# Kernel tuning notes

Measured on AMD Instinct MI355X. Metric: run time of the kernel, lower is better.

The kernel has to match this reference:

```python
import jax, jax.numpy as jnp
import numpy as np

N_NODES = 50000
N_EDGES = 1_600_000
DIMS = [512, 2048, 1024, 512]  # input, hiddens..., output
NEG_SLOPE = 0.2
EPS = 1e-12


def setup_inputs() -> dict:
    key = jax.random.key(0)
    ks = jax.random.split(key, 12)
    inp = {
        "x": jax.random.normal(ks[0], (N_NODES, DIMS[0]), dtype=jnp.float32),
        "edge_row": jax.random.randint(ks[1], (N_EDGES,), 0, N_NODES, dtype=jnp.int32),
        "edge_col": jax.random.randint(ks[2], (N_EDGES,), 0, N_NODES, dtype=jnp.int32),
        "edge_val": jax.random.uniform(ks[3], (N_EDGES,), dtype=jnp.float32),
    }
    # GraphConvolution params per layer: W [d_in, d_out], b [d_out]
    for i in range(len(DIMS) - 1):
        d_in, d_out = DIMS[i], DIMS[i + 1]
        scale = 1.0 / np.sqrt(d_in)
        inp[f"W{i}"] = jax.random.uniform(ks[4 + 2 * i], (d_in, d_out), minval=-scale, maxval=scale, dtype=jnp.float32)
        inp[f"b{i}"] = jnp.zeros((d_out,), dtype=jnp.float32)
    return inp


def _spmm(edge_row, edge_col, edge_val, h):
    # out[i] = sum_{e: row[e]==i} val[e] * h[col[e]]   (sparse adj @ h)
    msgs = edge_val[:, None] * h[edge_col]  # [E, d]
    return jax.ops.segment_sum(msgs, edge_row, num_segments=N_NODES)


def reference(x, edge_row, edge_col, edge_val, W0, b0, W1, b1, W2, b2):
    Ws = [W0, W1, W2]
    bs = [b0, b1, b2]
    # F.normalize: L2-normalize each row
    norm = jnp.sqrt(jnp.sum(x * x, axis=1, keepdims=True))
    h = x / jnp.maximum(norm, EPS)
    n_layers = len(Ws)
    for i in range(n_layers):
        support = h @ Ws[i]                                  # [N, d_out]
        h = _spmm(edge_row, edge_col, edge_val, support) + bs[i]
        if i != n_layers - 1:
            # dropout is identity at inference; leaky_relu(0.2)
            h = jnp.where(h >= 0, h, NEG_SLOPE * h)
    return h
```

## Files before the change

### kernel.cpp

```cpp
#include <hip/hip_runtime.h>
#include <stdint.h>

#define N_NODES 50000
#define N_EDGES 1600000
#define NCB 13

typedef __attribute__((ext_vector_type(8))) short bf16x8;
typedef __attribute__((ext_vector_type(4))) float f32x4;
typedef __attribute__((ext_vector_type(8))) unsigned short u16x8;

__device__ __forceinline__ float b2f(unsigned short u) {
  union { unsigned int i; float f; } v; v.i = ((unsigned int)u) << 16; return v.f;
}
__device__ __forceinline__ unsigned short f2b(float f) {
  union { float f; unsigned int i; } v; v.f = f;
  unsigned int u = v.i;
  u += 0x7fffu + ((u >> 16) & 1u);
  return (unsigned short)(u >> 16);
}

__device__ __forceinline__ void load_lds16(const void* g, void* l) {
  __builtin_amdgcn_global_load_lds(
      (const __attribute__((address_space(1))) unsigned int*)g,
      (__attribute__((address_space(3))) unsigned int*)l, 16, 0, 0);
}

__global__ __launch_bounds__(256) void normalize_k(const float* __restrict__ x,
                                                   unsigned short* __restrict__ out) {
  int lane = threadIdx.x & 63;
  int row = blockIdx.x * 4 + (threadIdx.x >> 6);
  const float* p = x + (size_t)row * 512 + lane * 8;
  float4 a = ((const float4*)p)[0];
  float4 b = ((const float4*)p)[1];
  float ss = a.x*a.x + a.y*a.y + a.z*a.z + a.w*a.w
           + b.x*b.x + b.y*b.y + b.z*b.z + b.w*b.w;
#pragma unroll
  for (int off = 1; off < 64; off <<= 1) ss += __shfl_xor(ss, off, 64);
  float s = 1.0f / fmaxf(sqrtf(ss), 1e-12f);
  u16x8 o;
  o[0]=f2b(a.x*s); o[1]=f2b(a.y*s); o[2]=f2b(a.z*s); o[3]=f2b(a.w*s);
  o[4]=f2b(b.x*s); o[5]=f2b(b.y*s); o[6]=f2b(b.z*s); o[7]=f2b(b.w*s);
  *(u16x8*)(out + (size_t)row * 512 + lane * 8) = o;
}

__global__ __launch_bounds__(256) void hist2_k(const int* __restrict__ er, const int* __restrict__ ec,
                                               int* __restrict__ h2) {
  int i = blockIdx.x * 256 + threadIdx.x;
  if (i < N_EDGES) atomicAdd(&h2[er[i] * NCB + (ec[i] >> 12)], 1);
}

__global__ __launch_bounds__(256) void scan1_k(const int* __restrict__ deg, int* __restrict__ out,
                                               int* __restrict__ csum, int n) {
  __shared__ int sd[256];
  int t = threadIdx.x;
  int base = blockIdx.x * 1024;
  int v[4], s = 0;
#pragma unroll
  for (int j = 0; j < 4; ++j) {
    int idx = base + t * 4 + j;
    v[j] = (idx < n) ? deg[idx] : 0;
    s += v[j];
  }
  sd[t] = s;
  __syncthreads();
  for (int off = 1; off < 256; off <<= 1) {
    int xx = (t >= off) ? sd[t - off] : 0;
    __syncthreads();
    sd[t] += xx;
    __syncthreads();
  }
  if (t == 255) csum[blockIdx.x] = sd[255];
  int run = sd[t] - s;
#pragma unroll
  for (int j = 0; j < 4; ++j) {
    int idx = base + t * 4 + j;
    if (idx < n) out[idx] = run;
    run += v[j];
  }
}

__global__ __launch_bounds__(256) void scan2p_k(int* __restrict__ csum, int n) {
  __shared__ int sd[256];
  int t = threadIdx.x;
  int v[3], s = 0;
#pragma unroll
  for (int j = 0; j < 3; ++j) {
    int idx = t * 3 + j;
    v[j] = (idx < n) ? csum[idx] : 0;
    s += v[j];
  }
  sd[t] = s;
  __syncthreads();
  for (int off = 1; off < 256; off <<= 1) {
    int xx = (t >= off) ? sd[t - off] : 0;
    __syncthreads();
    sd[t] += xx;
    __syncthreads();
  }
  int run = sd[t] - s;
#pragma unroll
  for (int j = 0; j < 3; ++j) {
    int idx = t * 3 + j;
    if (idx < n) csum[idx] = run;
    run += v[j];
  }
}

__global__ __launch_bounds__(256) void scan3_k(int* __restrict__ out, const int* __restrict__ csum, int n) {
  int i = blockIdx.x * 256 + threadIdx.x;
  if (i < n) out[i] += csum[i >> 10];
}

__global__ __launch_bounds__(256) void extract_k(const int* __restrict__ rs2, int* __restrict__ rs_s) {
  int i = blockIdx.x * 256 + threadIdx.x;
  if (i < N_NODES) rs_s[i] = rs2[i * NCB];
  if (i == N_NODES) rs_s[i] = N_EDGES;
}

__global__ __launch_bounds__(256) void scatter2_k(const int* __restrict__ er, const int* __restrict__ ec,
    const float* __restrict__ ev, int* __restrict__ head2, int2* __restrict__ ep) {
  int i = blockIdx.x * 256 + threadIdx.x;
  if (i < N_EDGES) {
    int r = er[i], c = ec[i];
    int p = atomicAdd(&head2[r * NCB + (c >> 12)], 1);
    ep[p] = make_int2(c, __float_as_int(ev[i]));
  }
}

__global__ __launch_bounds__(256) void wconv_k(const float* __restrict__ W,
                                               unsigned short* __restrict__ WT, int K, int N) {
  int i = blockIdx.x * 256 + threadIdx.x;
  if (i < N * K) {
    int n = i / K, k = i - n * K;
    WT[i] = f2b(W[(size_t)k * N + n]);
  }
}

template <int D, int MODE>
__global__ __launch_bounds__(256) void spmm_k(const unsigned short* __restrict__ in,
    const int* __restrict__ rs, const int2* __restrict__ ep,
    const float* __restrict__ bias, void* __restrict__ outv) {
  constexpr int NS = D / 512;
  int lane = threadIdx.x & 63;
  int blk = blockIdx.x;
  int slice = (NS == 1) ? 0 : (blk / 12500);
  int rowg = (NS == 1) ? blk : (blk - slice * 12500);
  int row = rowg * 4 + (threadIdx.x >> 6);
  int e0 = rs[row];
  int e1 = rs[row + 1];
  float acc[8] = {0.f, 0.f, 0.f, 0.f, 0.f, 0.f, 0.f, 0.f};
  const unsigned short* base = in + (size_t)slice * 512 + (size_t)lane * 8;
  int e = e0;
  for (; e + 4 <= e1; e += 4) {
    int2 p0 = ep[e];
    int2 p1 = ep[e + 1];
    int2 p2 = ep[e + 2];
    int2 p3 = ep[e + 3];
    unsigned c0 = (unsigned)p0.x < N_NODES ? (unsigned)p0.x : 0u;
    unsigned c1 = (unsigned)p1.x < N_NODES ? (unsigned)p1.x : 0u;
    unsigned c2 = (unsigned)p2.x < N_NODES ? (unsigned)p2.x : 0u;
    unsigned c3 = (unsigned)p3.x < N_NODES ? (unsigned)p3.x : 0u;
    u16x8 u0 = *(const u16x8*)(base + (size_t)c0 * D);
    u16x8 u1 = *(const u16x8*)(base + (size_t)c1 * D);
    u16x8 u2 = *(const u16x8*)(base + (size_t)c2 * D);
    u16x8 u3 = *(const u16x8*)(base + (size_t)c3 * D);
    float v0 = __int_as_float(p0.y), v1 = __int_as_float(p1.y);
    float v2 = __int_as_float(p2.y), v3 = __int_as_float(p3.y);
#pragma unroll
    for (int h = 0; h < 8; ++h) acc[h] = fmaf(v0, b2f(u0[h]), acc[h]);
#pragma unroll
    for (int h = 0; h < 8; ++h) acc[h] = fmaf(v1, b2f(u1[h]), acc[h]);
#pragma unroll
    for (int h = 0; h < 8; ++h) acc[h] = fmaf(v2, b2f(u2[h]), acc[h]);
#pragma unroll
    for (int h = 0; h < 8; ++h) acc[h] = fmaf(v3, b2f(u3[h]), acc[h]);
  }
  for (; e < e1; ++e) {
    int2 p = ep[e];
    unsigned c = (unsigned)p.x < N_NODES ? (unsigned)p.x : 0u;
    u16x8 u = *(const u16x8*)(base + (size_t)c * D);
    float v = __int_as_float(p.y);
#pragma unroll
    for (int h = 0; h < 8; ++h) acc[h] = fmaf(v, b2f(u[h]), acc[h]);
  }
  size_t obase = (size_t)row * D + (size_t)slice * 512 + lane * 8;
  int bbase = slice * 512 + lane * 8;
  if (MODE == 2) {
    float* out = (float*)outv;
#pragma unroll
    for (int j = 0; j < 8; ++j) out[obase + j] = acc[j] + bias[bbase + j];
  } else {
    unsigned short* out = (unsigned short*)outv;
    u16x8 o;
#pragma unroll
    for (int h = 0; h < 8; ++h) {
      float xo = acc[h];
      if (MODE == 1) {
        xo += bias[bbase + h];
        xo = xo >= 0.f ? xo : 0.2f * xo;
      }
      o[h] = f2b(xo);
    }
    *(u16x8*)(out + obase) = o;
  }
}

template <bool BIAS_RELU>
__global__ __launch_bounds__(256) void gemm_bt_k(
    const unsigned short* __restrict__ A, const unsigned short* __restrict__ BT,
    const float* __restrict__ bias, unsigned short* __restrict__ C,
    int M, int N, int K) {
  __shared__ __align__(16) unsigned short sA[128 * 32];
  __shared__ __align__(16) unsigned short sB[128 * 32];
  int tid = threadIdx.x;
  int lane = tid & 63;
  int wid = tid >> 6;
  int wm = (wid & 1) * 64;
  int wn = (wid >> 1) * 64;
  int mblk = blockIdx.y * 128;
  int nblk = blockIdx.x * 128;
  const unsigned short* Bb = BT + (size_t)nblk * K;
  int c0 = tid, c1 = tid + 256;
  int ar0 = c0 >> 2, ac0 = (c0 & 3) * 8;
  int ar1 = c1 >> 2, ac1 = (c1 & 3) * 8;
  int ra0 = mblk + ar0; if (ra0 > M - 1) ra0 = M - 1;
  int ra1 = mblk + ar1; if (ra1 > M - 1) ra1 = M - 1;
  f32x4 acc[4][4] = {};
  for (int k0 = 0; k0 < K; k0 += 32) {
    load_lds16(A + (size_t)ra0 * K + k0 + ac0, &sA[c0 * 8]);
    load_lds16(A + (size_t)ra1 * K + k0 + ac1, &sA[c1 * 8]);
    load_lds16(Bb + (size_t)ar0 * K + k0 + ac0, &sB[c0 * 8]);
    load_lds16(Bb + (size_t)ar1 * K + k0 + ac1, &sB[c1 * 8]);
    __syncthreads();
    bf16x8 af[4], bfr[4];
    int kq = (lane >> 4) * 8;
    int mr = wm + (lane & 15);
    int nr = wn + (lane & 15);
#pragma unroll
    for (int i = 0; i < 4; ++i) af[i] = *(const bf16x8*)&sA[(mr + i * 16) * 32 + kq];
#pragma unroll
    for (int j = 0; j < 4; ++j) bfr[j] = *(const bf16x8*)&sB[(nr + j * 16) * 32 + kq];
#pragma unroll
    for (int i = 0; i < 4; ++i)
#pragma unroll
      for (int j = 0; j < 4; ++j)
        acc[i][j] = __builtin_amdgcn_mfma_f32_16x16x32_bf16(af[i], bfr[j], acc[i][j], 0, 0, 0);
    __syncthreads();
  }
  int quad = lane >> 4;
  int lc = lane & 15;
#pragma unroll
  for (int i = 0; i < 4; ++i) {
#pragma unroll
    for (int r = 0; r < 4; ++r) {
      int gm = mblk + wm + i * 16 + quad * 4 + r;
      if (gm < M) {
#pragma unroll
        for (int j = 0; j < 4; ++j) {
          int gn = nblk + wn + j * 16 + lc;
          float v = acc[i][j][r];
          if (BIAS_RELU) { v += bias[gn]; v = v >= 0.f ? v : 0.2f * v; }
          C[(size_t)gm * N + gn] = f2b(v);
        }
      }
    }
  }
}

extern "C" void kernel_launch(void* const* d_in, const int* in_sizes, int n_in,
                              void* d_out, int out_size, void* d_ws, size_t ws_size,
                              hipStream_t stream) {
  (void)in_sizes; (void)n_in; (void)out_size;
  const float* x  = (const float*)d_in[0];
  const int* erow = (const int*)d_in[1];
  const int* ecol = (const int*)d_in[2];
  const float* ev = (const float*)d_in[3];
  const float* W0 = (const float*)d_in[4];
  const float* b0 = (const float*)d_in[5];
  const float* W1 = (const float*)d_in[6];
  const float* b1 = (const float*)d_in[7];
  const float* W2 = (const float*)d_in[8];
  const float* b2 = (const float*)d_in[9];

  const size_t POOL_T1 = 256000000;
  const size_t POOL_T2 = 204800000;
  const size_t POOL_T3 = 153600000;
  const size_t META = 12800000 + 200064 + 7340032;
  int tier = (ws_size >= POOL_T1 + META) ? 1 : (ws_size >= POOL_T2 + META) ? 2 : 3;
  size_t pool_sz = (tier == 1) ? POOL_T1 : (tier == 2) ? POOL_T2 : POOL_T3;

  char* ws = (char*)d_ws;
  int2*  ep   = (int2*)(ws + pool_sz);
  int*   rs_s = (int*)(ws + pool_sz + 12800000);
  unsigned short* w0t = (unsigned short*)(ws + pool_sz + 12800000 + 200064);
  unsigned short* w1t = w0t + (size_t)2048 * 512;
  unsigned short* w2t = w1t + (size_t)1024 * 2048;
  int* rs2   = (int*)(ws);
  int* csum  = (int*)(ws + 2600064);
  int* head2 = (int*)(ws + 2604160);
  unsigned short* u = (unsigned short*)d_out;

  hipMemsetAsync(rs2, 0, 2600064, stream);
  hist2_k<<<6250, 256, 0, stream>>>(erow, ecol, rs2);
  scan1_k<<<635, 256, 0, stream>>>(rs2, rs2, csum, N_NODES * NCB);
  scan2p_k<<<1, 256, 0, stream>>>(csum, 635);
  scan3_k<<<2540, 256, 0, stream>>>(rs2, csum, N_NODES * NCB);
  extract_k<<<196, 256, 0, stream>>>(rs2, rs_s);
  hipMemcpyAsync(head2, rs2, (size_t)N_NODES * NCB * 4, hipMemcpyDeviceToDevice, stream);
  scatter2_k<<<6250, 256, 0, stream>>>(erow, ecol, ev, head2, ep);

  wconv_k<<<4096, 256, 0, stream>>>(W0, w0t, 512, 2048);
  wconv_k<<<8192, 256, 0, stream>>>(W1, w1t, 2048, 1024);
  wconv_k<<<2048, 256, 0, stream>>>(W2, w2t, 1024, 512);

  if (tier == 1) {
    unsigned short* h1        = (unsigned short*)(ws);
    unsigned short* norm_out  = (unsigned short*)(ws);
    unsigned short* spmm0_out = (unsigned short*)(ws + 204800000);
    unsigned short* h2        = (unsigned short*)(ws);
    unsigned short* vbuf      = (unsigned short*)(ws + 102400000);
    normalize_k<<<12500, 256, 0, stream>>>(x, norm_out);
    spmm_k<512, 0><<<12500, 256, 0, stream>>>(norm_out, rs_s, ep, nullptr, spmm0_out);
    gemm_bt_k<true ><<<dim3(16, 391), 256, 0, stream>>>(spmm0_out, w0t, b0, h1, N_NODES, 2048, 512);
    gemm_bt_k<false><<<dim3(8, 391), 256, 0, stream>>>(h1, w1t, nullptr, u, N_NODES, 1024, 2048);
    spmm_k<1024, 1><<<25000, 256, 0, stream>>>(u, rs_s, ep, b1, h2);
    gemm_bt_k<false><<<dim3(4, 391), 256, 0, stream>>>(h2, w2t, nullptr, vbuf, N_NODES, 512, 1024);
    spmm_k<512, 2><<<12500, 256, 0, stream>>>(vbuf, rs_s, ep, b2, (float*)d_out);
  } else {
    int nchunk = (tier == 2) ? 2 : 4;
    int crows = (tier == 2) ? 25000 : 12500;
    int ytiles = (tier == 2) ? 196 : 98;
    unsigned short* norm_out  = (unsigned short*)(ws);
    unsigned short* spmm0_out = (unsigned short*)(ws + 51200000);
    unsigned short* h1chunk   = (unsigned short*)(ws + 102400000);
    unsigned short* h2        = (unsigned short*)(ws);
    unsigned short* vbuf      = (unsigned short*)(ws + 102400000);
    normalize_k<<<12500, 256, 0, stream>>>(x, norm_out);
    spmm_k<512, 0><<<12500, 256, 0, stream>>>(norm_out, rs_s, ep, nullptr, spmm0_out);
    for (int c = 0; c < nchunk; ++c) {
      const unsigned short* a0 = spmm0_out + (size_t)c * crows * 512;
      unsigned short* uc = u + (size_t)c * crows * 1024;
      gemm_bt_k<true ><<<dim3(16, ytiles), 256, 0, stream>>>(a0, w0t, b0, h1chunk, crows, 2048, 512);
      gemm_bt_k<false><<<dim3(8, ytiles), 256, 0, stream>>>(h1chunk, w1t, nullptr, uc, crows, 1024, 2048);
    }
    spmm_k<1024, 1><<<25000, 256, 0, stream>>>(u, rs_s, ep, b1, h2);
    gemm_bt_k<false><<<dim3(4, 391), 256, 0, stream>>>(h2, w2t, nullptr, vbuf, N_NODES, 512, 1024);
    spmm_k<512, 2><<<12500, 256, 0, stream>>>(vbuf, rs_s, ep, b2, (float*)d_out);
  }
}
```

Before: 1.831 ms.

## Refine column bucketing and restructure SpMM kernels with paired edge loads

Narrows the column bins used to sort edges within each row from 4096 to 2048 columns (NCB 13→25), aiming for better gather locality, and resizes the scan kernels and workspace offsets to match. The SpMM kernel is split into dedicated 512- and 1024-wide versions. Both read edge pairs with 16-byte aligned loads, and the 1024 version handles both halves of a row in one wave, so it runs half as many blocks and reads the edge list once instead of twice. Outputs are written with nontemporal stores. The cost is larger histogram and scan arrays plus more complex alignment peeling.

```diff
diff --git a/kernel.cpp b/kernel.cpp
--- a/kernel.cpp
+++ b/kernel.cpp
@@ -3,7 +3,8 @@
 
 #define N_NODES 50000
 #define N_EDGES 1600000
-#define NCB 13
+#define NCB 25
+#define CSHIFT 11
 
 typedef __attribute__((ext_vector_type(8))) short bf16x8;
 typedef __attribute__((ext_vector_type(4))) float f32x4;
@@ -23,6 +24,11 @@
   __builtin_amdgcn_global_load_lds(
       (const __attribute__((address_space(1))) unsigned int*)g,
       (__attribute__((address_space(3))) unsigned int*)l, 16, 0, 0);
+}
+
+__device__ __forceinline__ void fma8(float* acc, u16x8 u, float v) {
+#pragma unroll
+  for (int h = 0; h < 8; ++h) acc[h] = fmaf(v, b2f(u[h]), acc[h]);
 }
 
 __global__ __launch_bounds__(256) void normalize_k(const float* __restrict__ x,
@@ -46,7 +52,7 @@
 __global__ __launch_bounds__(256) void hist2_k(const int* __restrict__ er, const int* __restrict__ ec,
                                                int* __restrict__ h2) {
   int i = blockIdx.x * 256 + threadIdx.x;
-  if (i < N_EDGES) atomicAdd(&h2[er[i] * NCB + (ec[i] >> 12)], 1);
+  if (i < N_EDGES) atomicAdd(&h2[er[i] * NCB + (ec[i] >> CSHIFT)], 1);
 }
 
 __global__ __launch_bounds__(256) void scan1_k(const int* __restrict__ deg, int* __restrict__ out,
@@ -82,10 +88,10 @@
 __global__ __launch_bounds__(256) void scan2p_k(int* __restrict__ csum, int n) {
   __shared__ int sd[256];
   int t = threadIdx.x;
-  int v[3], s = 0;
-#pragma unroll
-  for (int j = 0; j < 3; ++j) {
-    int idx = t * 3 + j;
+  int v[5], s = 0;
+#pragma unroll
+  for (int j = 0; j < 5; ++j) {
+    int idx = t * 5 + j;
     v[j] = (idx < n) ? csum[idx] : 0;
     s += v[j];
   }
@@ -99,8 +105,8 @@
   }
   int run = sd[t] - s;
 #pragma unroll
-  for (int j = 0; j < 3; ++j) {
-    int idx = t * 3 + j;
+  for (int j = 0; j < 5; ++j) {
+    int idx = t * 5 + j;
     if (idx < n) csum[idx] = run;
     run += v[j];
   }
@@ -122,7 +128,7 @@
   int i = blockIdx.x * 256 + threadIdx.x;
   if (i < N_EDGES) {
     int r = er[i], c = ec[i];
-    int p = atomicAdd(&head2[r * NCB + (c >> 12)], 1);
+    int p = atomicAdd(&head2[r * NCB + (c >> CSHIFT)], 1);
     ep[p] = make_int2(c, __float_as_int(ev[i]));
   }
 }
@@ -136,73 +142,131 @@
   }
 }
 
-template <int D, int MODE>
-__global__ __launch_bounds__(256) void spmm_k(const unsigned short* __restrict__ in,
+template <int MODE>
+__global__ __launch_bounds__(256) void spmm512_k(const unsigned short* __restrict__ in,
     const int* __restrict__ rs, const int2* __restrict__ ep,
     const float* __restrict__ bias, void* __restrict__ outv) {
-  constexpr int NS = D / 512;
   int lane = threadIdx.x & 63;
-  int blk = blockIdx.x;
-  int slice = (NS == 1) ? 0 : (blk / 12500);
-  int rowg = (NS == 1) ? blk : (blk - slice * 12500);
-  int row = rowg * 4 + (threadIdx.x >> 6);
+  int row = blockIdx.x * 4 + (threadIdx.x >> 6);
   int e0 = rs[row];
   int e1 = rs[row + 1];
   float acc[8] = {0.f, 0.f, 0.f, 0.f, 0.f, 0.f, 0.f, 0.f};
-  const unsigned short* base = in + (size_t)slice * 512 + (size_t)lane * 8;
+  const unsigned short* base = in + (size_t)lane * 8;
   int e = e0;
+  if ((e & 1) && e < e1) {
+    int2 p = ep[e];
+    unsigned c = (unsigned)p.x < N_NODES ? (unsigned)p.x : 0u;
+    u16x8 u = *(const u16x8*)(base + (size_t)c * 512);
+    fma8(acc, u, __int_as_float(p.y));
+    ++e;
+  }
   for (; e + 4 <= e1; e += 4) {
-    int2 p0 = ep[e];
-    int2 p1 = ep[e + 1];
-    int2 p2 = ep[e + 2];
-    int2 p3 = ep[e + 3];
-    unsigned c0 = (unsigned)p0.x < N_NODES ? (unsigned)p0.x : 0u;
-    unsigned c1 = (unsigned)p1.x < N_NODES ? (unsigned)p1.x : 0u;
-    unsigned c2 = (unsigned)p2.x < N_NODES ? (unsigned)p2.x : 0u;
-    unsigned c3 = (unsigned)p3.x < N_NODES ? (unsigned)p3.x : 0u;
-    u16x8 u0 = *(const u16x8*)(base + (size_t)c0 * D);
-    u16x8 u1 = *(const u16x8*)(base + (size_t)c1 * D);
-    u16x8 u2 = *(const u16x8*)(base + (size_t)c2 * D);
-    u16x8 u3 = *(const u16x8*)(base + (size_t)c3 * D);
-    float v0 = __int_as_float(p0.y), v1 = __int_as_float(p1.y);
-    float v2 = __int_as_float(p2.y), v3 = __int_as_float(p3.y);
-#pragma unroll
-    for (int h = 0; h < 8; ++h) acc[h] = fmaf(v0, b2f(u0[h]), acc[h]);
-#pragma unroll
-    for (int h = 0; h < 8; ++h) acc[h] = fmaf(v1, b2f(u1[h]), acc[h]);
-#pragma unroll
-    for (int h = 0; h < 8; ++h) acc[h] = fmaf(v2, b2f(u2[h]), acc[h]);
-#pragma unroll
-    for (int h = 0; h < 8; ++h) acc[h] = fmaf(v3, b2f(u3[h]), acc[h]);
+    int4 q0 = *(const int4*)(&ep[e]);
+    int4 q1 = *(const int4*)(&ep[e + 2]);
+    unsigned c0 = (unsigned)q0.x < N_NODES ? (unsigned)q0.x : 0u;
+    unsigned c1 = (unsigned)q0.z < N_NODES ? (unsigned)q0.z : 0u;
+    unsigned c2 = (unsigned)q1.x < N_NODES ? (unsigned)q1.x : 0u;
+    unsigned c3 = (unsigned)q1.z < N_NODES ? (unsigned)q1.z : 0u;
+    u16x8 u0 = *(const u16x8*)(base + (size_t)c0 * 512);
+    u16x8 u1 = *(const u16x8*)(base + (size_t)c1 * 512);
+    u16x8 u2 = *(const u16x8*)(base + (size_t)c2 * 512);
+    u16x8 u3 = *(const u16x8*)(base + (size_t)c3 * 512);
+    fma8(acc, u0, __int_as_float(q0.y));
+    fma8(acc, u1, __int_as_float(q0.w));
+    fma8(acc, u2, __int_as_float(q1.y));
+    fma8(acc, u3, __int_as_float(q1.w));
   }
   for (; e < e1; ++e) {
     int2 p = ep[e];
     unsigned c = (unsigned)p.x < N_NODES ? (unsigned)p.x : 0u;
-    u16x8 u = *(const u16x8*)(base + (size_t)c * D);
-    float v = __int_as_float(p.y);
-#pragma unroll
-    for (int h = 0; h < 8; ++h) acc[h] = fmaf(v, b2f(u[h]), acc[h]);
-  }
-  size_t obase = (size_t)row * D + (size_t)slice * 512 + lane * 8;
-  int bbase = slice * 512 + lane * 8;
+    u16x8 u = *(const u16x8*)(base + (size_t)c * 512);
+    fma8(acc, u, __int_as_float(p.y));
+  }
+  size_t obase = (size_t)row * 512 + lane * 8;
   if (MODE == 2) {
     float* out = (float*)outv;
-#pragma unroll
-    for (int j = 0; j < 8; ++j) out[obase + j] = acc[j] + bias[bbase + j];
+    int bb = lane * 8;
+    f32x4 o0, o1;
+#pragma unroll
+    for (int j = 0; j < 4; ++j) o0[j] = acc[j] + bias[bb + j];
+#pragma unroll
+    for (int j = 0; j < 4; ++j) o1[j] = acc[4 + j] + bias[bb + 4 + j];
+    __builtin_nontemporal_store(o0, (f32x4*)(out + obase));
+    __builtin_nontemporal_store(o1, (f32x4*)(out + obase + 4));
   } else {
     unsigned short* out = (unsigned short*)outv;
     u16x8 o;
 #pragma unroll
-    for (int h = 0; h < 8; ++h) {
-      float xo = acc[h];
-      if (MODE == 1) {
-        xo += bias[bbase + h];
-        xo = xo >= 0.f ? xo : 0.2f * xo;
-      }
-      o[h] = f2b(xo);
-    }
-    *(u16x8*)(out + obase) = o;
-  }
+    for (int h = 0; h < 8; ++h) o[h] = f2b(acc[h]);
+    __builtin_nontemporal_store(o, (u16x8*)(out + obase));
+  }
+}
+
+__global__ __launch_bounds__(256) void spmm1024_k(const unsigned short* __restrict__ in,
+    const int* __restrict__ rs, const int2* __restrict__ ep,
+    const float* __restrict__ bias, unsigned short* __restrict__ out) {
+  int lane = threadIdx.x & 63;
+  int row = blockIdx.x * 4 + (threadIdx.x >> 6);
+  int e0 = rs[row];
+  int e1 = rs[row + 1];
+  float a0[8] = {0.f, 0.f, 0.f, 0.f, 0.f, 0.f, 0.f, 0.f};
+  float a1[8] = {0.f, 0.f, 0.f, 0.f, 0.f, 0.f, 0.f, 0.f};
+  const unsigned short* base = in + (size_t)lane * 8;
+  int e = e0;
+  if ((e & 1) && e < e1) {
+    int2 p = ep[e];
+    unsigned c = (unsigned)p.x < N_NODES ? (unsigned)p.x : 0u;
+    const unsigned short* r = base + (size_t)c * 1024;
+    u16x8 x0 = *(const u16x8*)r;
+    u16x8 x1 = *(const u16x8*)(r + 512);
+    float v = __int_as_float(p.y);
+    fma8(a0, x0, v);
+    fma8(a1, x1, v);
+    ++e;
+  }
+  for (; e + 2 <= e1; e += 2) {
+    int4 q = *(const int4*)(&ep[e]);
+    unsigned c0 = (unsigned)q.x < N_NODES ? (unsigned)q.x : 0u;
+    unsigned c1 = (unsigned)q.z < N_NODES ? (unsigned)q.z : 0u;
+    const unsigned short* r0 = base + (size_t)c0 * 1024;
+    const unsigned short* r1 = base + (size_t)c1 * 1024;
+    u16x8 x0 = *(const u16x8*)r0;
+    u16x8 x1 = *(const u16x8*)(r0 + 512);
+    u16x8 y0 = *(const u16x8*)r1;
+    u16x8 y1 = *(const u16x8*)(r1 + 512);
+    float v0 = __int_as_float(q.y), v1 = __int_as_float(q.w);
+    fma8(a0, x0, v0);
+    fma8(a1, x1, v0);
+    fma8(a0, y0, v1);
+    fma8(a1, y1, v1);
+  }
+  if (e < e1) {
+    int2 p = ep[e];
+    unsigned c = (unsigned)p.x < N_NODES ? (unsigned)p.x : 0u;
+    const unsigned short* r = base + (size_t)c * 1024;
+    u16x8 x0 = *(const u16x8*)r;
+    u16x8 x1 = *(const u16x8*)(r + 512);
+    float v = __int_as_float(p.y);
+    fma8(a0, x0, v);
+    fma8(a1, x1, v);
+  }
+  int bb = lane * 8;
+  u16x8 o0, o1;
+#pragma unroll
+  for (int h = 0; h < 8; ++h) {
+    float x = a0[h] + bias[bb + h];
+    x = x >= 0.f ? x : 0.2f * x;
+    o0[h] = f2b(x);
+  }
+#pragma unroll
+  for (int h = 0; h < 8; ++h) {
+    float x = a1[h] + bias[512 + bb + h];
+    x = x >= 0.f ? x : 0.2f * x;
+    o1[h] = f2b(x);
+  }
+  size_t ob = (size_t)row * 1024 + bb;
+  __builtin_nontemporal_store(o0, (u16x8*)(out + ob));
+  __builtin_nontemporal_store(o1, (u16x8*)(out + ob + 512));
 }
 
 template <bool BIAS_RELU>
@@ -296,17 +360,18 @@
   unsigned short* w1t = w0t + (size_t)2048 * 512;
   unsigned short* w2t = w1t + (size_t)1024 * 2048;
   int* rs2   = (int*)(ws);
-  int* csum  = (int*)(ws + 2600064);
-  int* head2 = (int*)(ws + 2604160);
+  int* csum  = (int*)(ws + 5000064);
+  int* head2 = (int*)(ws + 5008384);
   unsigned short* u = (unsigned short*)d_out;
 
-  hipMemsetAsync(rs2, 0, 2600064, stream);
+  const int NBIN = N_NODES * NCB;
+  hipMemsetAsync(rs2, 0, (size_t)NBIN * 4, stream);
   hist2_k<<<6250, 256, 0, stream>>>(erow, ecol, rs2);
-  scan1_k<<<635, 256, 0, stream>>>(rs2, rs2, csum, N_NODES * NCB);
-  scan2p_k<<<1, 256, 0, stream>>>(csum, 635);
-  scan3_k<<<2540, 256, 0, stream>>>(rs2, csum, N_NODES * NCB);
+  scan1_k<<<1221, 256, 0, stream>>>(rs2, rs2, csum, NBIN);
+  scan2p_k<<<1, 256, 0, stream>>>(csum, 1221);
+  scan3_k<<<4883, 256, 0, stream>>>(rs2, csum, NBIN);
   extract_k<<<196, 256, 0, stream>>>(rs2, rs_s);
-  hipMemcpyAsync(head2, rs2, (size_t)N_NODES * NCB * 4, hipMemcpyDeviceToDevice, stream);
+  hipMemcpyAsync(head2, rs2, (size_t)NBIN * 4, hipMemcpyDeviceToDevice, stream);
   scatter2_k<<<6250, 256, 0, stream>>>(erow, ecol, ev, head2, ep);
 
   wconv_k<<<4096, 256, 0, stream>>>(W0, w0t, 512, 2048);
@@ -320,12 +385,12 @@
     unsigned short* h2        = (unsigned short*)(ws);
     unsigned short* vbuf      = (unsigned short*)(ws + 102400000);
     normalize_k<<<12500, 256, 0, stream>>>(x, norm_out);
-    spmm_k<512, 0><<<12500, 256, 0, stream>>>(norm_out, rs_s, ep, nullptr, spmm0_out);
+    spmm512_k<0><<<12500, 256, 0, stream>>>(norm_out, rs_s, ep, nullptr, spmm0_out);
     gemm_bt_k<true ><<<dim3(16, 391), 256, 0, stream>>>(spmm0_out, w0t, b0, h1, N_NODES, 2048, 512);
     gemm_bt_k<false><<<dim3(8, 391), 256, 0, stream>>>(h1, w1t, nullptr, u, N_NODES, 1024, 2048);
-    spmm_k<1024, 1><<<25000, 256, 0, stream>>>(u, rs_s, ep, b1, h2);
+    spmm1024_k<<<12500, 256, 0, stream>>>(u, rs_s, ep, b1, h2);
     gemm_bt_k<false><<<dim3(4, 391), 256, 0, stream>>>(h2, w2t, nullptr, vbuf, N_NODES, 512, 1024);
-    spmm_k<512, 2><<<12500, 256, 0, stream>>>(vbuf, rs_s, ep, b2, (float*)d_out);
+    spmm512_k<2><<<12500, 256, 0, stream>>>(vbuf, rs_s, ep, b2, (float*)d_out);
   } else {
     int nchunk = (tier == 2) ? 2 : 4;
     int crows = (tier == 2) ? 25000 : 12500;
@@ -336,15 +401,15 @@
     unsigned short* h2        = (unsigned short*)(ws);
     unsigned short* vbuf      = (unsigned short*)(ws + 102400000);
     normalize_k<<<12500, 256, 0, stream>>>(x, norm_out);
-    spmm_k<512, 0><<<12500, 256, 0, stream>>>(norm_out, rs_s, ep, nullptr, spmm0_out);
+    spmm512_k<0><<<12500, 256, 0, stream>>>(norm_out, rs_s, ep, nullptr, spmm0_out);
     for (int c = 0; c < nchunk; ++c) {
       const unsigned short* a0 = spmm0_out + (size_t)c * crows * 512;
       unsigned short* uc = u + (size_t)c * crows * 1024;
       gemm_bt_k<true ><<<dim3(16, ytiles), 256, 0, stream>>>(a0, w0t, b0, h1chunk, crows, 2048, 512);
       gemm_bt_k<false><<<dim3(8, ytiles), 256, 0, stream>>>(h1chunk, w1t, nullptr, uc, crows, 1024, 2048);
     }
-    spmm_k<1024, 1><<<25000, 256, 0, stream>>>(u, rs_s, ep, b1, h2);
+    spmm1024_k<<<12500, 256, 0, stream>>>(u, rs_s, ep, b1, h2);
     gemm_bt_k<false><<<dim3(4, 391), 256, 0, stream>>>(h2, w2t, nullptr, vbuf, N_NODES, 512, 1024);
-    spmm_k<512, 2><<<12500, 256, 0, stream>>>(vbuf, rs_s, ep, b2, (float*)d_out);
-  }
-}
+    spmm512_k<2><<<12500, 256, 0, stream>>>(vbuf, rs_s, ep, b2, (float*)d_out);
+  }
+}
```

Result: slower. 1.900 ms (+3.8%).
